# Optimization experiments

Measured on AMD Instinct MI355X. Metric: run time of the kernel, lower is better.

The kernel has to match this reference:

```python
import math
import jax, jax.numpy as jnp
import numpy as np

B, S, D, H = 4, 2048, 1024, 16
DK = D // H


def setup_inputs() -> dict:
    key = jax.random.key(0)
    kx, kq, kk, kv, ko = jax.random.split(key, 5)
    scale = 1.0 / math.sqrt(D)
    return {
        "x": jax.random.normal(kx, (B, S, D), dtype=jnp.float32),
        "wq": jax.random.normal(kq, (D, D), dtype=jnp.float32) * scale,
        "wk": jax.random.normal(kk, (D, D), dtype=jnp.float32) * scale,
        "wv": jax.random.normal(kv, (D, D), dtype=jnp.float32) * scale,
        "wo": jax.random.normal(ko, (D, D), dtype=jnp.float32) * scale,
    }


def reference(x, wq, wk, wv, wo):
    b, s, d = x.shape
    # projections -> [b, h, s, dk]
    def split_heads(t):
        return t.reshape(b, s, H, DK).transpose(0, 2, 1, 3)
    q = split_heads(x @ wq)
    k = split_heads(x @ wk)
    v = split_heads(x @ wv)
    # scores [b, h, s, s], scaled by sqrt(d_k)
    scores = jnp.einsum('bhqd,bhkd->bhqk', q, k) / math.sqrt(DK)
    causal = jnp.tril(jnp.ones((s, s), dtype=bool))  # [s, s]
    scores = jnp.where(causal[None, None, :, :], scores, -jnp.inf)
    weights = jax.nn.softmax(scores, axis=-1)
    weights = jnp.nan_to_num(weights, nan=0.0)
    attn = jnp.einsum('bhqk,bhkd->bhqd', weights, v)
    attn = attn.transpose(0, 2, 1, 3).reshape(b, s, d)
    return attn @ wo
```

## Files before the change

### kernel.cpp

```cpp
#include <hip/hip_runtime.h>
#include <hip/hip_bf16.h>
#include <math.h>

#define B_ 4
#define S_ 2048
#define D_ 1024
#define H_ 16
#define DK_ 64

typedef __bf16 bf16;
typedef bf16 bf16x8 __attribute__((ext_vector_type(8)));
typedef float f32x4 __attribute__((ext_vector_type(4)));
typedef float f32x16 __attribute__((ext_vector_type(16)));

__device__ __forceinline__ int swz8(int row, int slot) {
    return row * 64 + ((slot ^ (row & 7)) << 3);
}
__device__ __forceinline__ unsigned packbf(float a, float b) {
    union { bf16 h[2]; unsigned u; } x;
    x.h[0] = (bf16)a; x.h[1] = (bf16)b;
    return x.u;
}
__device__ __forceinline__ void permswap(unsigned& x, unsigned& y) {
    asm("v_permlane32_swap_b32 %0, %1" : "+v"(x), "+v"(y));
}
__device__ __forceinline__ float fexp2(float x) {
#if __has_builtin(__builtin_amdgcn_exp2f)
    return __builtin_amdgcn_exp2f(x);
#else
    float r;
    asm("v_exp_f32 %0, %1" : "=v"(r) : "v"(x));
    return r;
#endif
}
__device__ __forceinline__ void gld16(bf16* lbase, const bf16* gsrc) {
    __builtin_amdgcn_global_load_lds(
        (const __attribute__((address_space(1))) unsigned*)gsrc,
        (__attribute__((address_space(3))) unsigned*)lbase, 16, 0, 0);
}

__global__ __launch_bounds__(256) void prep_kernel(const float* __restrict__ x,
                                                   const float* __restrict__ wq, const float* __restrict__ wk,
                                                   const float* __restrict__ wv, const float* __restrict__ wo,
                                                   bf16* __restrict__ xb, bf16* __restrict__ wqkvT,
                                                   bf16* __restrict__ woT) {
    __shared__ float t[32][33];
    const int bid = blockIdx.x;
    const int tid = threadIdx.x;
    if (bid < 4096) {
        const size_t i = ((size_t)bid * 256 + tid) * 8;
        const float4* src = (const float4*)(x + i);
        float4 f0 = src[0], f1 = src[1];
        bf16x8 v;
        v[0] = (bf16)f0.x; v[1] = (bf16)f0.y; v[2] = (bf16)f0.z; v[3] = (bf16)f0.w;
        v[4] = (bf16)f1.x; v[5] = (bf16)f1.y; v[6] = (bf16)f1.z; v[7] = (bf16)f1.w;
        *(bf16x8*)(xb + i) = v;
    } else {
        const int b2 = bid - 4096;
        const int z = b2 >> 10;
        const float* src = (z == 0) ? wq : (z == 1) ? wk : (z == 2) ? wv : wo;
        bf16* dst = (z < 3) ? (wqkvT + (size_t)z * 1024 * 1024) : woT;
        const int n0 = (b2 & 31) * 32, k0 = ((b2 >> 5) & 31) * 32;
        const int tx = tid & 31, ty = tid >> 5;
#pragma unroll
        for (int j = 0; j < 4; ++j)
            t[ty + j * 8][tx] = src[(size_t)(k0 + ty + j * 8) * 1024 + n0 + tx];
        __syncthreads();
#pragma unroll
        for (int j = 0; j < 4; ++j)
            dst[(size_t)(n0 + ty + j * 8) * 1024 + k0 + tx] = (bf16)t[tx][ty + j * 8];
    }
}

__global__ __launch_bounds__(512) void gemm_qkv_kernel(const bf16* __restrict__ A, const bf16* __restrict__ Bt,
                                                       bf16* __restrict__ Qb, bf16* __restrict__ Kb,
                                                       bf16* __restrict__ Vt) {
    __shared__ __align__(16) bf16 As[128 * 64];
    __shared__ __align__(16) bf16 Bs[192 * 64];
    const int tid = threadIdx.x;
    const int lane = tid & 63;
    const int w = tid >> 6;
    const int wm = w >> 2, wn = w & 3;
    const int g = lane >> 4, r16 = lane & 15;

    const int bid = blockIdx.x;
    const int wg = (bid & 7) * 128 + (bid >> 3);
    const int mt = wg >> 4, nt = wg & 15;
    const int m0 = mt * 128, n0 = nt * 192;

    const int srow = tid >> 3;
    const int sslot = (tid & 7) ^ (srow & 7);
    const bf16* ga = A + (size_t)(m0 + srow) * 1024 + sslot * 8;
    const bf16* gb = Bt + (size_t)(n0 + srow) * 1024 + sslot * 8;
    const int wbase = w * 512;

    f32x4 acc[4][3] = {};

    for (int kt = 0; kt < 1024; kt += 64) {
#pragma unroll
        for (int p = 0; p < 2; ++p)
            gld16(&As[p * 4096 + wbase], ga + (size_t)p * 64 * 1024 + kt);
#pragma unroll
        for (int p = 0; p < 3; ++p)
            gld16(&Bs[p * 4096 + wbase], gb + (size_t)p * 64 * 1024 + kt);
        __syncthreads();
#pragma unroll
        for (int k0 = 0; k0 < 2; ++k0) {
            bf16x8 af[4], bfr[3];
#pragma unroll
            for (int mf = 0; mf < 4; ++mf)
                af[mf] = *(const bf16x8*)&As[swz8(wm * 64 + mf * 16 + r16, 4 * k0 + g)];
#pragma unroll
            for (int nf = 0; nf < 3; ++nf)
                bfr[nf] = *(const bf16x8*)&Bs[swz8(wn * 48 + nf * 16 + r16, 4 * k0 + g)];
#pragma unroll
            for (int mf = 0; mf < 4; ++mf)
#pragma unroll
                for (int nf = 0; nf < 3; ++nf)
                    acc[mf][nf] = __builtin_amdgcn_mfma_f32_16x16x32_bf16(af[mf], bfr[nf], acc[mf][nf], 0, 0, 0);
        }
        __syncthreads();
    }

#pragma unroll
    for (int mf = 0; mf < 4; ++mf) {
#pragma unroll
        for (int nf = 0; nf < 3; ++nf) {
            const int col = n0 + wn * 48 + nf * 16 + r16;
            const int seg = col >> 10;
            const int n1 = col & 1023;
            const int h = n1 >> 6, dk = n1 & 63;
            const int row0 = m0 + wm * 64 + mf * 16 + 4 * g;
            const int b = row0 >> 11, s0 = row0 & 2047;
            if (seg == 2) {
                union { bf16 h4[4]; unsigned long long u; } pk;
#pragma unroll
                for (int rr = 0; rr < 4; ++rr) pk.h4[rr] = (bf16)acc[mf][nf][rr];
                *(unsigned long long*)(Vt + (((size_t)b * H_ + h) * DK_ + dk) * S_ + s0) = pk.u;
            } else {
                bf16* dst = (seg == 0) ? Qb : Kb;
#pragma unroll
                for (int rr = 0; rr < 4; ++rr)
                    dst[(((size_t)b * H_ + h) * S_ + s0 + rr) * DK_ + dk] = (bf16)acc[mf][nf][rr];
            }
        }
    }
}

__global__ __launch_bounds__(256) void gemm_out_kernel(const bf16* __restrict__ A, const bf16* __restrict__ Bt,
                                                       float* __restrict__ o0, int M, int N, int K, int NT) {
    __shared__ __align__(16) bf16 As[128 * 64];
    __shared__ __align__(16) bf16 Bs[128 * 64];
    const int tid = threadIdx.x;
    const int lane = tid & 63;
    const int w = tid >> 6;
    const int wm = w >> 1, wn = w & 1;
    const int g = lane >> 4, r16 = lane & 15;

    const int bid = blockIdx.x;
    const int qch = gridDim.x >> 3;
    const int wg = (bid & 7) * qch + (bid >> 3);
    const int mt = wg / NT, nt = wg % NT;
    const int m0 = mt * 128, n0 = nt * 128;

    const int srow = tid >> 3;
    const int sslot = (tid & 7) ^ (srow & 7);
    const bf16* ga = A + (size_t)(m0 + srow) * K + sslot * 8;
    const bf16* gb = Bt + (size_t)(n0 + srow) * K + sslot * 8;

    f32x4 acc[4][4] = {};

    for (int kt = 0; kt < K; kt += 64) {
#pragma unroll
        for (int p = 0; p < 4; ++p) {
            gld16(&As[p * 2048 + w * 512], ga + (size_t)p * 32 * K + kt);
            gld16(&Bs[p * 2048 + w * 512], gb + (size_t)p * 32 * K + kt);
        }
        __syncthreads();
#pragma unroll
        for (int k0 = 0; k0 < 2; ++k0) {
            bf16x8 af[4], bfr[4];
#pragma unroll
            for (int mf = 0; mf < 4; ++mf)
                af[mf] = *(const bf16x8*)&As[swz8(wm * 64 + mf * 16 + r16, 4 * k0 + g)];
#pragma unroll
            for (int nf = 0; nf < 4; ++nf)
                bfr[nf] = *(const bf16x8*)&Bs[swz8(wn * 64 + nf * 16 + r16, 4 * k0 + g)];
#pragma unroll
            for (int mf = 0; mf < 4; ++mf)
#pragma unroll
                for (int nf = 0; nf < 4; ++nf)
                    acc[mf][nf] = __builtin_amdgcn_mfma_f32_16x16x32_bf16(af[mf], bfr[nf], acc[mf][nf], 0, 0, 0);
        }
        __syncthreads();
    }

#pragma unroll
    for (int mf = 0; mf < 4; ++mf)
#pragma unroll
        for (int nf = 0; nf < 4; ++nf)
#pragma unroll
            for (int rr = 0; rr < 4; ++rr) {
                int row = m0 + wm * 64 + mf * 16 + 4 * g + rr;
                int col = n0 + wn * 64 + nf * 16 + r16;
                o0[(size_t)row * N + col] = acc[mf][nf][rr];
            }
}

__global__ __launch_bounds__(256, 4) void attn_kernel(const bf16* __restrict__ Q,
                                                      const bf16* __restrict__ Kb,
                                                      const bf16* __restrict__ Vt,
                                                      bf16* __restrict__ ctx) {
    __shared__ __align__(16) bf16 lds[4][4096];
    const int bh = blockIdx.x;
    const int QTBL[16] = {15, 14, 13, 12, 0, 1, 2, 3, 11, 10, 9, 8, 4, 5, 6, 7};
    const int qt = QTBL[blockIdx.y];
    const int tid = threadIdx.x;
    const int lane = tid & 63, w = tid >> 6;
    const int lq = lane & 31, hi = lane >> 5;
    const int q0 = qt * 128;
    const int q0w = q0 + w * 32;
    const int q = q0w + lq;
    const int njt = 2 * qt + 2;
    const float qscale = 0.125f * 1.44269504088896340736f;

    const int srow = tid >> 3;
    const int sslot = (tid & 7) ^ (srow & 7);
    const bf16* kg = Kb + ((size_t)bh * S_ + srow) * DK_ + sslot * 8;
    const bf16* vg = Vt + ((size_t)bh * DK_ + srow) * S_ + sslot * 8;

    bf16x8 qf[4];
    {
        const bf16* qp = Q + ((size_t)bh * S_ + q) * DK_ + hi * 8;
#pragma unroll
        for (int kc = 0; kc < 4; ++kc) {
            bf16x8 raw = *(const bf16x8*)(qp + kc * 16);
#pragma unroll
            for (int e = 0; e < 8; ++e) qf[kc][e] = (bf16)((float)raw[e] * qscale);
        }
    }

    f32x16 accd[2] = {};
    float lsum = 0.f;

    bf16x8 kreg0 = *(const bf16x8*)kg;
    bf16x8 kreg1 = *(const bf16x8*)(kg + 32 * DK_);
    bf16x8 vreg0 = *(const bf16x8*)vg;
    bf16x8 vreg1 = *(const bf16x8*)(vg + 32 * S_);

    for (int jt = 0; jt < njt; ++jt) {
        const int cur = jt & 1;
        *(bf16x8*)&lds[cur][tid * 8] = kreg0;
        *(bf16x8*)&lds[cur][tid * 8 + 2048] = kreg1;
        *(bf16x8*)&lds[2 + cur][tid * 8] = vreg0;
        *(bf16x8*)&lds[2 + cur][tid * 8 + 2048] = vreg1;
        if (jt + 1 < njt) {
            kreg0 = *(const bf16x8*)(kg + (size_t)(jt + 1) * 64 * DK_);
            kreg1 = *(const bf16x8*)(kg + (size_t)(jt + 1) * 64 * DK_ + 32 * DK_);
            vreg0 = *(const bf16x8*)(vg + (jt + 1) * 64);
            vreg1 = *(const bf16x8*)(vg + (jt + 1) * 64 + 32 * S_);
        }
        __syncthreads();

        if (jt * 64 <= q0w + 31) {
            f32x16 sacc[2];
#pragma unroll
            for (int c = 0; c < 2; ++c)
#pragma unroll
                for (int r = 0; r < 16; ++r) sacc[c][r] = -16.0f;
            __builtin_amdgcn_s_setprio(1);
#pragma unroll
            for (int kc = 0; kc < 4; ++kc) {
#pragma unroll
                for (int c = 0; c < 2; ++c) {
                    bf16x8 kf = *(const bf16x8*)&lds[cur][swz8(c * 32 + lq, kc * 2 + hi)];
                    sacc[c] = __builtin_amdgcn_mfma_f32_32x32x16_bf16(kf, qf[kc], sacc[c], 0, 0, 0);
                }
            }
            __builtin_amdgcn_s_setprio(0);

            if (jt * 64 + 63 > q0w) {
#pragma unroll
                for (int c = 0; c < 2; ++c)
#pragma unroll
                    for (int r = 0; r < 16; ++r) {
                        int key = jt * 64 + c * 32 + (r & 3) + 8 * (r >> 2) + 4 * hi;
                        if (key > q) sacc[c][r] = -INFINITY;
                    }
            }

#pragma unroll
            for (int c = 0; c < 2; ++c)
#pragma unroll
                for (int r = 0; r < 16; ++r) sacc[c][r] = fexp2(sacc[c][r]);

            float s8[8];
#pragma unroll
            for (int i = 0; i < 8; ++i)
                s8[i] = (sacc[0][i] + sacc[0][i + 8]) + (sacc[1][i] + sacc[1][i + 8]);
#pragma unroll
            for (int i = 0; i < 4; ++i) s8[i] += s8[i + 4];
            lsum += (s8[0] + s8[1]) + (s8[2] + s8[3]);

#pragma unroll
            for (int kc = 0; kc < 4; ++kc) {
                const int c = kc >> 1, kf2 = kc & 1;
                unsigned w0 = packbf(sacc[c][8 * kf2 + 0], sacc[c][8 * kf2 + 1]);
                unsigned w1 = packbf(sacc[c][8 * kf2 + 2], sacc[c][8 * kf2 + 3]);
                unsigned w2 = packbf(sacc[c][8 * kf2 + 4], sacc[c][8 * kf2 + 5]);
                unsigned w3 = packbf(sacc[c][8 * kf2 + 6], sacc[c][8 * kf2 + 7]);
                permswap(w0, w2);
                permswap(w1, w3);
                union { unsigned wd[4]; bf16x8 v; } u;
                u.wd[0] = w0; u.wd[1] = w1; u.wd[2] = w2; u.wd[3] = w3;
                __builtin_amdgcn_s_setprio(1);
#pragma unroll
                for (int dt = 0; dt < 2; ++dt) {
                    bf16x8 vf = *(const bf16x8*)&lds[2 + cur][swz8(dt * 32 + lq, kc * 2 + hi)];
                    accd[dt] = __builtin_amdgcn_mfma_f32_32x32x16_bf16(vf, u.v, accd[dt], 0, 0, 0);
                }
                __builtin_amdgcn_s_setprio(0);
            }
        }
    }

    __syncthreads();
    bf16* eb = &lds[0][0];
    const float rl = 1.0f / (lsum + __shfl_xor(lsum, 32));
    {
        const int rowb = (w * 32 + lq) * 128;
        const int rsw = (lq & 7) << 4;
#pragma unroll
        for (int dt = 0; dt < 2; ++dt)
#pragma unroll
            for (int rq = 0; rq < 4; ++rq) {
                union { bf16 h[4]; unsigned long long u64; } pk;
#pragma unroll
                for (int j = 0; j < 4; ++j) pk.h[j] = (bf16)(accd[dt][rq * 4 + j] * rl);
                int off = rowb + ((dt * 64 + rq * 16 + hi * 8) ^ rsw);
                *(unsigned long long*)((char*)eb + off) = pk.u64;
            }
    }
    __syncthreads();
    {
        const int row = tid >> 1, half = tid & 1;
        const int b = bh >> 4, h = bh & 15;
        bf16* op = ctx + ((size_t)b * S_ + q0 + row) * D_ + h * DK_ + half * 32;
#pragma unroll
        for (int i = 0; i < 4; ++i) {
            int sl = half * 4 + i;
            int sls = sl ^ (row & 7);
            bf16x8 v = *(const bf16x8*)((const char*)eb + row * 128 + sls * 16);
            *(bf16x8*)(op + i * 8) = v;
        }
    }
}

extern "C" void kernel_launch(void* const* d_in, const int* in_sizes, int n_in,
                              void* d_out, int out_size, void* d_ws, size_t ws_size,
                              hipStream_t stream) {
    const float* x  = (const float*)d_in[0];
    const float* wq = (const float*)d_in[1];
    const float* wk = (const float*)d_in[2];
    const float* wv = (const float*)d_in[3];
    const float* wo = (const float*)d_in[4];

    char* ws = (char*)d_ws;
    bf16* wqkvT = (bf16*)(ws);
    bf16* woT   = (bf16*)(ws + 6291456);
    bf16* Qb    = (bf16*)(ws + 8388608);
    bf16* Kb    = (bf16*)(ws + 25165824);
    bf16* Vtb   = (bf16*)(ws + 58720256);
    bf16* ctx   = (bf16*)(ws + 75497472);
    bf16* xb    = ctx;

    prep_kernel<<<8192, 256, 0, stream>>>(x, wq, wk, wv, wo, xb, wqkvT, woT);
    gemm_qkv_kernel<<<1024, 512, 0, stream>>>(xb, wqkvT, Qb, Kb, Vtb);
    attn_kernel<<<dim3(64, 16), 256, 0, stream>>>(Qb, Kb, Vtb, ctx);
    gemm_out_kernel<<<512, 256, 0, stream>>>(ctx, woT, (float*)d_out, 8192, 1024, 1024, 8);
}
```

Measured before the change: 143.9 us.

## Fold softmax scale into Wq and enlarge output GEMM tile to 256x128

```diff
diff --git a/kernel.cpp b/kernel.cpp
--- a/kernel.cpp
+++ b/kernel.cpp
@@ -60,6 +60,7 @@
         const int z = b2 >> 10;
         const float* src = (z == 0) ? wq : (z == 1) ? wk : (z == 2) ? wv : wo;
         bf16* dst = (z < 3) ? (wqkvT + (size_t)z * 1024 * 1024) : woT;
+        const float s = (z == 0) ? (0.125f * 1.44269504088896340736f) : 1.0f;
         const int n0 = (b2 & 31) * 32, k0 = ((b2 >> 5) & 31) * 32;
         const int tx = tid & 31, ty = tid >> 5;
 #pragma unroll
@@ -68,7 +69,7 @@
         __syncthreads();
 #pragma unroll
         for (int j = 0; j < 4; ++j)
-            dst[(size_t)(n0 + ty + j * 8) * 1024 + k0 + tx] = (bf16)t[tx][ty + j * 8];
+            dst[(size_t)(n0 + ty + j * 8) * 1024 + k0 + tx] = (bf16)(t[tx][ty + j * 8] * s);
     }
 }
 
@@ -147,63 +148,64 @@
     }
 }
 
-__global__ __launch_bounds__(256) void gemm_out_kernel(const bf16* __restrict__ A, const bf16* __restrict__ Bt,
-                                                       float* __restrict__ o0, int M, int N, int K, int NT) {
-    __shared__ __align__(16) bf16 As[128 * 64];
+__global__ __launch_bounds__(512) void gemm_out_kernel(const bf16* __restrict__ A, const bf16* __restrict__ Bt,
+                                                       float* __restrict__ o0) {
+    __shared__ __align__(16) bf16 As[256 * 64];
     __shared__ __align__(16) bf16 Bs[128 * 64];
     const int tid = threadIdx.x;
     const int lane = tid & 63;
     const int w = tid >> 6;
-    const int wm = w >> 1, wn = w & 1;
+    const int wm = w >> 2, wn = w & 3;
     const int g = lane >> 4, r16 = lane & 15;
 
     const int bid = blockIdx.x;
-    const int qch = gridDim.x >> 3;
-    const int wg = (bid & 7) * qch + (bid >> 3);
-    const int mt = wg / NT, nt = wg % NT;
-    const int m0 = mt * 128, n0 = nt * 128;
+    const int wg = (bid & 7) * 32 + (bid >> 3);
+    const int mt = wg >> 3, nt = wg & 7;
+    const int m0 = mt * 256, n0 = nt * 128;
 
     const int srow = tid >> 3;
     const int sslot = (tid & 7) ^ (srow & 7);
-    const bf16* ga = A + (size_t)(m0 + srow) * K + sslot * 8;
-    const bf16* gb = Bt + (size_t)(n0 + srow) * K + sslot * 8;
-
-    f32x4 acc[4][4] = {};
-
-    for (int kt = 0; kt < K; kt += 64) {
-#pragma unroll
-        for (int p = 0; p < 4; ++p) {
-            gld16(&As[p * 2048 + w * 512], ga + (size_t)p * 32 * K + kt);
-            gld16(&Bs[p * 2048 + w * 512], gb + (size_t)p * 32 * K + kt);
-        }
+    const bf16* ga = A + (size_t)(m0 + srow) * 1024 + sslot * 8;
+    const bf16* gb = Bt + (size_t)(n0 + srow) * 1024 + sslot * 8;
+    const int wbase = w * 512;
+
+    f32x4 acc[8][2] = {};
+
+    for (int kt = 0; kt < 1024; kt += 64) {
+#pragma unroll
+        for (int p = 0; p < 4; ++p)
+            gld16(&As[p * 4096 + wbase], ga + (size_t)p * 64 * 1024 + kt);
+#pragma unroll
+        for (int p = 0; p < 2; ++p)
+            gld16(&Bs[p * 4096 + wbase], gb + (size_t)p * 64 * 1024 + kt);
         __syncthreads();
 #pragma unroll
         for (int k0 = 0; k0 < 2; ++k0) {
-            bf16x8 af[4], bfr[4];
-#pragma unroll
-            for (int mf = 0; mf < 4; ++mf)
-                af[mf] = *(const bf16x8*)&As[swz8(wm * 64 + mf * 16 + r16, 4 * k0 + g)];
-#pragma unroll
-            for (int nf = 0; nf < 4; ++nf)
-                bfr[nf] = *(const bf16x8*)&Bs[swz8(wn * 64 + nf * 16 + r16, 4 * k0 + g)];
-#pragma unroll
-            for (int mf = 0; mf < 4; ++mf)
-#pragma unroll
-                for (int nf = 0; nf < 4; ++nf)
+            bf16x8 af[8], bfr[2];
+#pragma unroll
+            for (int mf = 0; mf < 8; ++mf)
+                af[mf] = *(const bf16x8*)&As[swz8(wm * 128 + mf * 16 + r16, 4 * k0 + g)];
+#pragma unroll
+            for (int nf = 0; nf < 2; ++nf)
+                bfr[nf] = *(const bf16x8*)&Bs[swz8(wn * 32 + nf * 16 + r16, 4 * k0 + g)];
+#pragma unroll
+            for (int mf = 0; mf < 8; ++mf)
+#pragma unroll
+                for (int nf = 0; nf < 2; ++nf)
                     acc[mf][nf] = __builtin_amdgcn_mfma_f32_16x16x32_bf16(af[mf], bfr[nf], acc[mf][nf], 0, 0, 0);
         }
         __syncthreads();
     }
 
 #pragma unroll
-    for (int mf = 0; mf < 4; ++mf)
-#pragma unroll
-        for (int nf = 0; nf < 4; ++nf)
+    for (int mf = 0; mf < 8; ++mf)
+#pragma unroll
+        for (int nf = 0; nf < 2; ++nf)
 #pragma unroll
             for (int rr = 0; rr < 4; ++rr) {
-                int row = m0 + wm * 64 + mf * 16 + 4 * g + rr;
-                int col = n0 + wn * 64 + nf * 16 + r16;
-                o0[(size_t)row * N + col] = acc[mf][nf][rr];
+                int row = m0 + wm * 128 + mf * 16 + 4 * g + rr;
+                int col = n0 + wn * 32 + nf * 16 + r16;
+                o0[(size_t)row * 1024 + col] = acc[mf][nf][rr];
             }
 }
 
@@ -222,7 +224,6 @@
     const int q0w = q0 + w * 32;
     const int q = q0w + lq;
     const int njt = 2 * qt + 2;
-    const float qscale = 0.125f * 1.44269504088896340736f;
 
     const int srow = tid >> 3;
     const int sslot = (tid & 7) ^ (srow & 7);
@@ -233,11 +234,7 @@
     {
         const bf16* qp = Q + ((size_t)bh * S_ + q) * DK_ + hi * 8;
 #pragma unroll
-        for (int kc = 0; kc < 4; ++kc) {
-            bf16x8 raw = *(const bf16x8*)(qp + kc * 16);
-#pragma unroll
-            for (int e = 0; e < 8; ++e) qf[kc][e] = (bf16)((float)raw[e] * qscale);
-        }
+        for (int kc = 0; kc < 4; ++kc) qf[kc] = *(const bf16x8*)(qp + kc * 16);
     }
 
     f32x16 accd[2] = {};
@@ -377,5 +374,5 @@
     prep_kernel<<<8192, 256, 0, stream>>>(x, wq, wk, wv, wo, xb, wqkvT, woT);
     gemm_qkv_kernel<<<1024, 512, 0, stream>>>(xb, wqkvT, Qb, Kb, Vtb);
     attn_kernel<<<dim3(64, 16), 256, 0, stream>>>(Qb, Kb, Vtb, ctx);
-    gemm_out_kernel<<<512, 256, 0, stream>>>(ctx, woT, (float*)d_out, 8192, 1024, 1024, 8);
-}
+    gemm_out_kernel<<<256, 512, 0, stream>>>(ctx, woT, (float*)d_out);
+}
```

Result: no change. 146.4 us (+1.7%).
